# Kernel optimization log

Measured on AMD Instinct MI355X. Metric: run time of the kernel, lower is better.

The kernel has to match this reference:

```python
import jax, jax.numpy as jnp
import numpy as np

N, E, CIN, COUT = 100000, 1600000, 64, 128
EPS = 1e-5  # torch BatchNorm default


def setup_inputs() -> dict:
    key = jax.random.key(0)
    ks = jax.random.split(key, 16)
    s = 0.1
    x = jax.random.normal(ks[0], (N, CIN), jnp.float32)
    src = jax.random.randint(ks[1], (E,), 0, N, dtype=jnp.int32)
    dst = jax.random.randint(ks[2], (E,), 0, N, dtype=jnp.int32)
    edge_index = jnp.stack([src, dst])  # [2, E]
    return {
        "x": x,
        "edge_index": edge_index,
        # conv0: GraphConv(CIN -> COUT)
        "W_root0": jax.random.normal(ks[3], (COUT, CIN), jnp.float32) * s,
        "W_nbr0": jax.random.normal(ks[4], (COUT, CIN), jnp.float32) * s,
        "b0": jnp.zeros((COUT,), jnp.float32),
        # bn0
        "g0": jnp.ones((COUT,), jnp.float32),
        "be0": jnp.zeros((COUT,), jnp.float32),
        # conv1: GraphConv(COUT -> COUT)
        "W_root1": jax.random.normal(ks[5], (COUT, COUT), jnp.float32) * s,
        "W_nbr1": jax.random.normal(ks[6], (COUT, COUT), jnp.float32) * s,
        "b1": jnp.zeros((COUT,), jnp.float32),
        # bn1
        "g1": jnp.ones((COUT,), jnp.float32),
        "be1": jnp.zeros((COUT,), jnp.float32),
        # residual 1x1 conv (Conv1d(CIN, COUT, 1))
        "Wlin": jax.random.normal(ks[7], (COUT, CIN), jnp.float32) * s,
        "blin": jnp.zeros((COUT,), jnp.float32),
    }


def graph_conv(x, src, dst, W_root, W_nbr, b):
    # PyG GraphConv: out_i = W_root x_i + W_nbr * sum_{j: (j->i) in E} x_j + b
    agg = jax.ops.segment_sum(x[src], dst, num_segments=N)  # scatter-add over edges
    return x @ W_root.T + agg @ W_nbr.T + b


def batch_norm(x, gamma, beta):
    # training-mode BatchNorm over the node dimension (biased variance)
    mu = jnp.mean(x, axis=0)
    var = jnp.mean(jnp.square(x - mu), axis=0)
    return (x - mu) * jax.lax.rsqrt(var + EPS) * gamma + beta


def reference(x, edge_index, W_root0, W_nbr0, b0, g0, be0,
              W_root1, W_nbr1, b1, g1, be1, Wlin, blin):
    src, dst = edge_index[0], edge_index[1]
    y = batch_norm(graph_conv(x, src, dst, W_root0, W_nbr0, b0), g0, be0)
    y = jax.nn.relu(y)
    y = batch_norm(graph_conv(y, src, dst, W_root1, W_nbr1, b1), g1, be1)
    out = y + (x @ Wlin.T + blin)  # 1x1 Conv1d residual projection
    return jax.nn.relu(out)
```

## Files before the change

### kernel.cpp

```cpp
#include <hip/hip_runtime.h>
#include <stdint.h>


#define CIN 64
#define COUT 128
#define BN_EPS 1e-5f
#define CURPAD 32
#define PCPAD 32
#define SPAD 32
#define PSH 10
#define PNODES (1 << PSH)
#define MAXP 128

typedef unsigned short u16;
typedef short short8 __attribute__((ext_vector_type(8)));
typedef float f32x4 __attribute__((ext_vector_type(4)));

__device__ __forceinline__ float bf2f(u16 u) {
    union { unsigned int i; float f; } v; v.i = ((unsigned int)u) << 16; return v.f;
}
__device__ __forceinline__ u16 f2bf(float f) {
    union { float f; unsigned int i; } v; v.f = f;
    unsigned int r = v.i + 0x7fffu + ((v.i >> 16) & 1u);
    return (u16)(r >> 16);
}
__device__ __forceinline__ float lo16(unsigned int w) { return bf2f((u16)(w & 0xffffu)); }
__device__ __forceinline__ float hi16(unsigned int w) { return bf2f((u16)(w >> 16)); }

template<bool BF> __device__ __forceinline__ float ldf(const void* p, long i) {
    if (BF) return bf2f(((const u16*)p)[i]);
    return ((const float*)p)[i];
}
template<bool BF> __device__ __forceinline__ short8 ld8(const void* p, long i) {
    if (BF) return *(const short8*)((const u16*)p + i);
    const float* f = (const float*)p + i;
    short8 r;
#pragma unroll
    for (int j = 0; j < 8; ++j) r[j] = (short)f2bf(f[j]);
    return r;
}

__global__ void k_detect(const unsigned int* __restrict__ x, int* __restrict__ flag) {
    int lane = threadIdx.x;
    int cnt = 0;
#pragma unroll
    for (int i = 0; i < 8; ++i) {
        unsigned int w = x[lane * 8 + i];
        unsigned int e0 = (w >> 7) & 0xFFu, e1 = (w >> 23) & 0xFFu;
        cnt += (e0 >= 0x60u && e0 <= 0x8Eu);
        cnt += (e1 >= 0x60u && e1 <= 0x8Eu);
    }
    for (int o = 32; o; o >>= 1) cnt += __shfl_down(cnt, o);
    if (lane == 0) *flag = (cnt > 850) ? 1 : 0;
}

__global__ __launch_bounds__(256) void k_phist(const int* __restrict__ dst,
                                               int* __restrict__ pcount, int E, int np) {
    __shared__ int h[MAXP];
    for (int i = threadIdx.x; i < np; i += 256) h[i] = 0;
    __syncthreads();
    int stride = gridDim.x * 256;
    for (int e = blockIdx.x * 256 + threadIdx.x; e < E; e += stride)
        atomicAdd(&h[dst[e] >> PSH], 1);
    __syncthreads();
    for (int i = threadIdx.x; i < np; i += 256)
        if (h[i]) atomicAdd(&pcount[i * PCPAD], h[i]);
}

__global__ void k_pscan(const int* __restrict__ pcount, int* __restrict__ pstart,
                        int* __restrict__ pcursor, int np, int E) {
    __shared__ int s[MAXP];
    int t = threadIdx.x;
    int v = (t < np) ? pcount[t * PCPAD] : 0;
    s[t] = v; __syncthreads();
    for (int o = 1; o < MAXP; o <<= 1) {
        int u = (t >= o) ? s[t - o] : 0;
        __syncthreads(); s[t] += u; __syncthreads();
    }
    if (t < np) {
        int ex = s[t] - v;
        pstart[t] = ex;
        pcursor[t * CURPAD] = ex;
    }
    if (t == 0) pstart[np] = E;
}

__global__ __launch_bounds__(256) void k_pfill(const int* __restrict__ src,
        const int* __restrict__ dst, int* __restrict__ pcursor,
        unsigned int* __restrict__ barr, int E, int np) {
    __shared__ int cnt[MAXP], gb[MAXP], loc[MAXP];
    int tid = threadIdx.x;
    int base = blockIdx.x * 4096;
    for (int i = tid; i < np; i += 256) { cnt[i] = 0; loc[i] = 0; }
    __syncthreads();
    int pk[16]; unsigned int rec[16];
#pragma unroll
    for (int k = 0; k < 16; ++k) {
        int e = base + k * 256 + tid;
        if (e < E) {
            int d = dst[e];
            pk[k] = d >> PSH;
            rec[k] = ((unsigned int)(d & (PNODES - 1)) << 20) | (unsigned int)src[e];
            atomicAdd(&cnt[pk[k]], 1);
        } else pk[k] = -1;
    }
    __syncthreads();
    for (int i = tid; i < np; i += 256)
        if (cnt[i]) gb[i] = atomicAdd(&pcursor[i * CURPAD], cnt[i]);
    __syncthreads();
#pragma unroll
    for (int k = 0; k < 16; ++k) {
        if (pk[k] >= 0) {
            int off = atomicAdd(&loc[pk[k]], 1);
            barr[gb[pk[k]] + off] = rec[k];
        }
    }
}

__global__ __launch_bounds__(256) void k_psort(const unsigned int* __restrict__ barr,
        const int* __restrict__ pstart, int* __restrict__ csr,
        int* __restrict__ row_start, int n, int np, int E) {
    __shared__ int hist[PNODES], curs[PNODES], tsum[256];
    int tid = threadIdx.x;
    int p = blockIdx.x;
    int e0 = pstart[p], e1 = pstart[p + 1];
    int node0 = p << PSH;
#pragma unroll
    for (int j = 0; j < PNODES / 256; ++j) hist[tid + j * 256] = 0;
    __syncthreads();
    for (int t = e0 + tid; t < e1; t += 256)
        atomicAdd(&hist[barr[t] >> 20], 1);
    __syncthreads();
    int s0 = hist[tid * 4], s1 = hist[tid * 4 + 1], s2 = hist[tid * 4 + 2], s3 = hist[tid * 4 + 3];
    int sum4 = s0 + s1 + s2 + s3;
    tsum[tid] = sum4; __syncthreads();
    for (int o = 1; o < 256; o <<= 1) {
        int u = (tid >= o) ? tsum[tid - o] : 0;
        __syncthreads(); tsum[tid] += u; __syncthreads();
    }
    int bexc = tsum[tid] - sum4;
    int off0 = bexc, off1 = bexc + s0, off2 = off1 + s1, off3 = off2 + s2;
    curs[tid * 4] = off0; curs[tid * 4 + 1] = off1;
    curs[tid * 4 + 2] = off2; curs[tid * 4 + 3] = off3;
    int nd = node0 + tid * 4;
    if (nd < n)     row_start[nd]     = e0 + off0;
    if (nd + 1 < n) row_start[nd + 1] = e0 + off1;
    if (nd + 2 < n) row_start[nd + 2] = e0 + off2;
    if (nd + 3 < n) row_start[nd + 3] = e0 + off3;
    if (p == np - 1 && tid == 0) row_start[n] = E;
    __syncthreads();
    for (int t = e0 + tid; t < e1; t += 256) {
        unsigned int rec = barr[t];
        int pos = atomicAdd(&curs[rec >> 20], 1);
        csr[e0 + pos] = (int)(rec & 0xFFFFF);
    }
}

template<bool BF>
__device__ __forceinline__ void agg0_impl(const void* x, const int* rs, const int* csr,
                                          u16* agg, int n) {
    int i = blockIdx.x * 4 + (threadIdx.x >> 6);
    if (i >= n) return;
    int lane = threadIdx.x & 63;
    int h = lane >> 5, cp = lane & 31;
    int b = rs[i], e = rs[i + 1];
    float a0 = 0.f, a1 = 0.f, b0 = 0.f, b1 = 0.f;
    int t = b + h;
    for (; t + 2 < e; t += 4) {
        int j0 = csr[t], j1 = csr[t + 2];
        if (BF) {
            unsigned int w0 = ((const unsigned int*)x)[(long)j0 * 32 + cp];
            unsigned int w1 = ((const unsigned int*)x)[(long)j1 * 32 + cp];
            a0 += lo16(w0); a1 += hi16(w0);
            b0 += lo16(w1); b1 += hi16(w1);
        } else {
            float2 w0 = ((const float2*)x)[(long)j0 * 32 + cp];
            float2 w1 = ((const float2*)x)[(long)j1 * 32 + cp];
            a0 += w0.x; a1 += w0.y;
            b0 += w1.x; b1 += w1.y;
        }
    }
    for (; t < e; t += 2) {
        int j0 = csr[t];
        if (BF) {
            unsigned int w0 = ((const unsigned int*)x)[(long)j0 * 32 + cp];
            a0 += lo16(w0); a1 += hi16(w0);
        } else {
            float2 w0 = ((const float2*)x)[(long)j0 * 32 + cp];
            a0 += w0.x; a1 += w0.y;
        }
    }
    a0 += b0; a1 += b1;
    a0 += __shfl_xor(a0, 32);
    a1 += __shfl_xor(a1, 32);
    if (h == 0) {
        unsigned int o = (unsigned int)f2bf(a0) | ((unsigned int)f2bf(a1) << 16);
        ((unsigned int*)agg)[(long)i * 32 + cp] = o;
    }
}

__global__ __launch_bounds__(256) void k_agg0(const int* __restrict__ flag,
        const void* x, const int* __restrict__ rs, const int* __restrict__ csr,
        u16* __restrict__ agg, int n) {
    if (*flag) agg0_impl<true >(x, rs, csr, agg, n);
    else       agg0_impl<false>(x, rs, csr, agg, n);
}

__global__ __launch_bounds__(256) void k_agg1(const u16* __restrict__ y0,
        const int* __restrict__ rs, const int* __restrict__ csr,
        const float* __restrict__ scale, const float* __restrict__ shift,
        u16* __restrict__ agg, int n) {
    int i = blockIdx.x * 4 + (threadIdx.x >> 6);
    if (i >= n) return;
    int lane = threadIdx.x & 63;
    int c0 = 2 * lane;
    float s0 = scale[c0], s1 = scale[c0 + 1];
    float h0 = shift[c0], h1 = shift[c0 + 1];
    const unsigned int* y32 = (const unsigned int*)y0;
    int b = rs[i], e = rs[i + 1];
    float a0 = 0.f, a1 = 0.f, b0 = 0.f, b1 = 0.f;
    float c0a = 0.f, c1a = 0.f, d0 = 0.f, d1 = 0.f;
    int t = b;
    for (; t + 4 <= e; t += 4) {
        int j0 = csr[t], j1 = csr[t + 1], j2 = csr[t + 2], j3 = csr[t + 3];
        unsigned int w0 = y32[(long)j0 * 64 + lane];
        unsigned int w1 = y32[(long)j1 * 64 + lane];
        unsigned int w2 = y32[(long)j2 * 64 + lane];
        unsigned int w3 = y32[(long)j3 * 64 + lane];
        a0  += fmaxf(lo16(w0) * s0 + h0, 0.f); a1  += fmaxf(hi16(w0) * s1 + h1, 0.f);
        b0  += fmaxf(lo16(w1) * s0 + h0, 0.f); b1  += fmaxf(hi16(w1) * s1 + h1, 0.f);
        c0a += fmaxf(lo16(w2) * s0 + h0, 0.f); c1a += fmaxf(hi16(w2) * s1 + h1, 0.f);
        d0  += fmaxf(lo16(w3) * s0 + h0, 0.f); d1  += fmaxf(hi16(w3) * s1 + h1, 0.f);
    }
    for (; t < e; ++t) {
        unsigned int w0 = y32[(long)csr[t] * 64 + lane];
        a0 += fmaxf(lo16(w0) * s0 + h0, 0.f); a1 += fmaxf(hi16(w0) * s1 + h1, 0.f);
    }
    float s0t = (a0 + b0) + (c0a + d0);
    float s1t = (a1 + b1) + (c1a + d1);
    ((unsigned int*)agg)[(long)i * 64 + lane] =
        (unsigned int)f2bf(s0t) | ((unsigned int)f2bf(s1t) << 16);
}

template<bool BF>
__device__ __forceinline__ void gemm0_impl(const void* x, const u16* agg,
                                           const void* Wr, const void* Wn,
                                           u16* y0, float* sumP, float* sqP,
                                           int n, int nch, u16* lds) {
    const int ST = 130;
    int tid = threadIdx.x;
    int wave = tid >> 6, lane = tid & 63, lr = lane & 15, q = lane >> 4;

    short8 wf[2][4];
#pragma unroll
    for (int i = 0; i < 2; ++i) {
        int c = (2 * wave + i) * 16 + lr;
#pragma unroll
        for (int ks = 0; ks < 4; ++ks) {
            const void* W = (ks < 2) ? Wr : Wn;
            wf[i][ks] = ld8<BF>(W, (long)c * CIN + (ks & 1) * 32 + q * 8);
        }
    }

    const int rowb = tid >> 3, wb = tid & 7;
    const int rowf = tid >> 4, wfc = tid & 15;
    short8 rbx[2]; float4 rfx[4]; short8 rag[2];

    auto regload = [&](long chunk0) {
        if (BF) {
#pragma unroll
            for (int i = 0; i < 2; ++i) {
                long rg = chunk0 + rowb + i * 32; if (rg > n - 1) rg = n - 1;
                rbx[i] = *(const short8*)((const u16*)x + rg * CIN + wb * 8);
            }
        } else {
#pragma unroll
            for (int i = 0; i < 4; ++i) {
                long rg = chunk0 + rowf + i * 16; if (rg > n - 1) rg = n - 1;
                rfx[i] = *(const float4*)((const float*)x + rg * CIN + wfc * 4);
            }
        }
#pragma unroll
        for (int i = 0; i < 2; ++i) {
            long rg = chunk0 + rowb + i * 32; if (rg > n - 1) rg = n - 1;
            rag[i] = *(const short8*)(agg + rg * CIN + wb * 8);
        }
    };

    float st[2] = {0.f, 0.f}, sq[2] = {0.f, 0.f};
    int ch = blockIdx.x;
    if (ch < nch) regload((long)ch * 64);
    for (; ch < nch; ch += gridDim.x) {
        long chunk0 = (long)ch * 64;
        __syncthreads();
        if (BF) {
#pragma unroll
            for (int i = 0; i < 2; ++i)
                *(short8*)(lds + (rowb + i * 32) * ST + wb * 8) = rbx[i];
        } else {
#pragma unroll
            for (int i = 0; i < 4; ++i) {
                u16* d = lds + (rowf + i * 16) * ST + wfc * 4;
                d[0] = f2bf(rfx[i].x); d[1] = f2bf(rfx[i].y);
                d[2] = f2bf(rfx[i].z); d[3] = f2bf(rfx[i].w);
            }
        }
#pragma unroll
        for (int i = 0; i < 2; ++i)
            *(short8*)(lds + (rowb + i * 32) * ST + 64 + wb * 8) = rag[i];
        __syncthreads();
        long nxt = (long)ch + gridDim.x;
        if (nxt < nch) regload(nxt * 64);

#pragma unroll
        for (int t = 0; t < 4; ++t) {
            short8 a[4];
#pragma unroll
            for (int ks = 0; ks < 4; ++ks)
                a[ks] = *(const short8*)(lds + (t * 16 + lr) * ST + ks * 32 + q * 8);
#pragma unroll
            for (int i = 0; i < 2; ++i) {
                f32x4 acc = {0.f, 0.f, 0.f, 0.f};
#pragma unroll
                for (int ks = 0; ks < 4; ++ks)
                    acc = __builtin_amdgcn_mfma_f32_16x16x32_bf16(a[ks], wf[i][ks], acc, 0, 0, 0);
                int c = (2 * wave + i) * 16 + lr;
#pragma unroll
                for (int r = 0; r < 4; ++r) {
                    long row = chunk0 + t * 16 + q * 4 + r;
                    if (row < n) {
                        y0[row * COUT + c] = f2bf(acc[r]);
                        st[i] += acc[r]; sq[i] += acc[r] * acc[r];
                    }
                }
            }
        }
    }
#pragma unroll
    for (int i = 0; i < 2; ++i) {
        st[i] += __shfl_xor(st[i], 16); st[i] += __shfl_xor(st[i], 32);
        sq[i] += __shfl_xor(sq[i], 16); sq[i] += __shfl_xor(sq[i], 32);
    }
    if (q == 0) {
#pragma unroll
        for (int i = 0; i < 2; ++i) {
            int c = (2 * wave + i) * 16 + lr;
            atomicAdd(&sumP[c * SPAD], st[i]);
            atomicAdd(&sqP[c * SPAD], sq[i]);
        }
    }
}

__global__ __launch_bounds__(256) void k_gemm0(const int* __restrict__ flag,
        const void* x, const u16* __restrict__ agg, const void* Wr, const void* Wn,
        u16* __restrict__ y0, float* __restrict__ sumP, float* __restrict__ sqP,
        int n, int nch) {
    __shared__ u16 lds[64 * 130];
    if (*flag) gemm0_impl<true >(x, agg, Wr, Wn, y0, sumP, sqP, n, nch, lds);
    else       gemm0_impl<false>(x, agg, Wr, Wn, y0, sumP, sqP, n, nch, lds);
}

template<bool BF>
__device__ __forceinline__ void gemm1_impl(const u16* y0, const u16* agg,
                                           const void* Wr, const void* Wn,
                                           const float* sc0, const float* sh0,
                                           u16* y1, float* sumP, float* sqP,
                                           int n, int nch, u16* lds) {
    const int ST = 258;
    int tid = threadIdx.x;
    int wave = tid >> 6, lane = tid & 63, lr = lane & 15, q = lane >> 4;

    short8 wf[2][8];
#pragma unroll
    for (int i = 0; i < 2; ++i) {
        int c = (2 * wave + i) * 16 + lr;
#pragma unroll
        for (int ks = 0; ks < 8; ++ks) {
            const void* W = (ks < 4) ? Wr : Wn;
            wf[i][ks] = ld8<BF>(W, (long)c * COUT + (ks & 3) * 32 + q * 8);
        }
    }

    const int rowy = tid >> 4, wy = tid & 15;
    float s8[8], h8[8];
#pragma unroll
    for (int j = 0; j < 8; ++j) { s8[j] = sc0[wy * 8 + j]; h8[j] = sh0[wy * 8 + j]; }

    short8 ry[4], rag[4];
    auto regload = [&](long chunk0) {
#pragma unroll
        for (int i = 0; i < 4; ++i) {
            long rg = chunk0 + rowy + i * 16; if (rg > n - 1) rg = n - 1;
            ry[i]  = *(const short8*)(y0  + rg * COUT + wy * 8);
            rag[i] = *(const short8*)(agg + rg * COUT + wy * 8);
        }
    };

    float st[2] = {0.f, 0.f}, sq[2] = {0.f, 0.f};
    int ch = blockIdx.x;
    if (ch < nch) regload((long)ch * 64);
    for (; ch < nch; ch += gridDim.x) {
        long chunk0 = (long)ch * 64;
        __syncthreads();
#pragma unroll
        for (int i = 0; i < 4; ++i) {
            short8 o;
#pragma unroll
            for (int j = 0; j < 8; ++j)
                o[j] = (short)f2bf(fmaxf(bf2f((u16)ry[i][j]) * s8[j] + h8[j], 0.f));
            *(short8*)(lds + (rowy + i * 16) * ST + wy * 8) = o;
            *(short8*)(lds + (rowy + i * 16) * ST + 128 + wy * 8) = rag[i];
        }
        __syncthreads();
        long nxt = (long)ch + gridDim.x;
        if (nxt < nch) regload(nxt * 64);

#pragma unroll
        for (int t = 0; t < 4; ++t) {
            short8 a[8];
#pragma unroll
            for (int ks = 0; ks < 8; ++ks)
                a[ks] = *(const short8*)(lds + (t * 16 + lr) * ST + ks * 32 + q * 8);
#pragma unroll
            for (int i = 0; i < 2; ++i) {
                f32x4 acc = {0.f, 0.f, 0.f, 0.f};
#pragma unroll
                for (int ks = 0; ks < 8; ++ks)
                    acc = __builtin_amdgcn_mfma_f32_16x16x32_bf16(a[ks], wf[i][ks], acc, 0, 0, 0);
                int c = (2 * wave + i) * 16 + lr;
#pragma unroll
                for (int r = 0; r < 4; ++r) {
                    long row = chunk0 + t * 16 + q * 4 + r;
                    if (row < n) {
                        y1[row * COUT + c] = f2bf(acc[r]);
                        st[i] += acc[r]; sq[i] += acc[r] * acc[r];
                    }
                }
            }
        }
    }
#pragma unroll
    for (int i = 0; i < 2; ++i) {
        st[i] += __shfl_xor(st[i], 16); st[i] += __shfl_xor(st[i], 32);
        sq[i] += __shfl_xor(sq[i], 16); sq[i] += __shfl_xor(sq[i], 32);
    }
    if (q == 0) {
#pragma unroll
        for (int i = 0; i < 2; ++i) {
            int c = (2 * wave + i) * 16 + lr;
            atomicAdd(&sumP[c * SPAD], st[i]);
            atomicAdd(&sqP[c * SPAD], sq[i]);
        }
    }
}

__global__ __launch_bounds__(256) void k_gemm1(const int* __restrict__ flag,
        const u16* __restrict__ y0, const u16* __restrict__ agg,
        const void* Wr, const void* Wn,
        const float* __restrict__ sc0, const float* __restrict__ sh0,
        u16* y1_bf , u16* y1_ws,
        float* __restrict__ sumP, float* __restrict__ sqP, int n, int nch) {
    __shared__ u16 lds[64 * 258];
    u16* y1 = *flag ? y1_bf : y1_ws;
    if (*flag) gemm1_impl<true >(y0, agg, Wr, Wn, sc0, sh0, y1, sumP, sqP, n, nch, lds);
    else       gemm1_impl<false>(y0, agg, Wr, Wn, sc0, sh0, y1, sumP, sqP, n, nch, lds);
}

__global__ void k_bnfin(const int* __restrict__ flag,
                        const float* __restrict__ sumP, const float* __restrict__ sqP,
                        const void* g, const void* be,
                        float* __restrict__ scale, float* __restrict__ shift, int n) {
    int c = threadIdx.x;
    bool bf = (*flag != 0);
    float inv = 1.f / (float)n;
    float mu = sumP[c * SPAD] * inv;
    float var = fmaxf(sqP[c * SPAD] * inv - mu * mu, 0.f);
    float gv = bf ? bf2f(((const u16*)g)[c]) : ((const float*)g)[c];
    float bv = bf ? bf2f(((const u16*)be)[c]) : ((const float*)be)[c];
    float sc = gv * rsqrtf(var + BN_EPS);
    scale[c] = sc;
    shift[c] = bv - mu * sc;
}

template<bool BF>
__device__ __forceinline__ void final_impl(const void* x, const u16* y1,
                                           const void* Wlin, const void* blin,
                                           const float* sc, const float* sh,
                                           void* out, int n, int nch, u16* lds) {
    const int ST = 194;
    int tid = threadIdx.x;
    int wave = tid >> 6, lane = tid & 63, lr = lane & 15, q = lane >> 4;

    short8 wf[2][2];
    float blc[2], scc[2], shc[2];
#pragma unroll
    for (int i = 0; i < 2; ++i) {
        int c = (2 * wave + i) * 16 + lr;
#pragma unroll
        for (int ks = 0; ks < 2; ++ks)
            wf[i][ks] = ld8<BF>(Wlin, (long)c * CIN + ks * 32 + q * 8);
        blc[i] = ldf<BF>(blin, c);
        scc[i] = sc[c]; shc[i] = sh[c];
    }

    const int rowb = tid >> 3, wb = tid & 7;
    const int rowf = tid >> 4, wfc = tid & 15;
    const int rowy = tid >> 4, wy = tid & 15;
    short8 rbx[2]; float4 rfx[4]; short8 ry[4];

    auto regload = [&](long chunk0) {
        if (BF) {
#pragma unroll
            for (int i = 0; i < 2; ++i) {
                long rg = chunk0 + rowb + i * 32; if (rg > n - 1) rg = n - 1;
                rbx[i] = *(const short8*)((const u16*)x + rg * CIN + wb * 8);
            }
        } else {
#pragma unroll
            for (int i = 0; i < 4; ++i) {
                long rg = chunk0 + rowf + i * 16; if (rg > n - 1) rg = n - 1;
                rfx[i] = *(const float4*)((const float*)x + rg * CIN + wfc * 4);
            }
        }
#pragma unroll
        for (int i = 0; i < 4; ++i) {
            long rg = chunk0 + rowy + i * 16; if (rg > n - 1) rg = n - 1;
            ry[i] = *(const short8*)(y1 + rg * COUT + wy * 8);
        }
    };

    int ch = blockIdx.x;
    if (ch < nch) regload((long)ch * 64);
    for (; ch < nch; ch += gridDim.x) {
        long chunk0 = (long)ch * 64;
        __syncthreads();
        if (BF) {
#pragma unroll
            for (int i = 0; i < 2; ++i)
                *(short8*)(lds + (rowb + i * 32) * ST + wb * 8) = rbx[i];
        } else {
#pragma unroll
            for (int i = 0; i < 4; ++i) {
                u16* d = lds + (rowf + i * 16) * ST + wfc * 4;
                d[0] = f2bf(rfx[i].x); d[1] = f2bf(rfx[i].y);
                d[2] = f2bf(rfx[i].z); d[3] = f2bf(rfx[i].w);
            }
        }
#pragma unroll
        for (int i = 0; i < 4; ++i)
            *(short8*)(lds + (rowy + i * 16) * ST + 64 + wy * 8) = ry[i];
        __syncthreads();
        long nxt = (long)ch + gridDim.x;
        if (nxt < nch) regload(nxt * 64);

#pragma unroll
        for (int t = 0; t < 4; ++t) {
            short8 a[2];
#pragma unroll
            for (int ks = 0; ks < 2; ++ks)
                a[ks] = *(const short8*)(lds + (t * 16 + lr) * ST + ks * 32 + q * 8);
#pragma unroll
            for (int i = 0; i < 2; ++i) {
                f32x4 acc = {0.f, 0.f, 0.f, 0.f};
                acc = __builtin_amdgcn_mfma_f32_16x16x32_bf16(a[0], wf[i][0], acc, 0, 0, 0);
                acc = __builtin_amdgcn_mfma_f32_16x16x32_bf16(a[1], wf[i][1], acc, 0, 0, 0);
                int c = (2 * wave + i) * 16 + lr;
#pragma unroll
                for (int r = 0; r < 4; ++r) {
                    long row = chunk0 + t * 16 + q * 4 + r;
                    if (row < n) {
                        float yv = bf2f(lds[(t * 16 + q * 4 + r) * ST + 64 + c]);
                        float v = acc[r] + blc[i] + yv * scc[i] + shc[i];
                        v = fmaxf(v, 0.f);
                        if (BF) ((u16*)out)[row * COUT + c] = f2bf(v);
                        else    ((float*)out)[row * COUT + c] = v;
                    }
                }
            }
        }
    }
}

__global__ __launch_bounds__(256) void k_final(const int* __restrict__ flag,
        const void* x, const void* Wlin, const void* blin,
        const u16* y1_bf , const u16* y1_ws,
        const float* __restrict__ sc, const float* __restrict__ sh,
        void* out, int n, int nch) {
    __shared__ u16 lds[64 * 194];
    const u16* y1 = *flag ? y1_bf : y1_ws;
    if (*flag) final_impl<true >(x, y1, Wlin, blin, sc, sh, out, n, nch, lds);
    else       final_impl<false>(x, y1, Wlin, blin, sc, sh, out, n, nch, lds);
}

extern "C" void kernel_launch(void* const* d_in, const int* in_sizes, int n_in,
                              void* d_out, int out_size, void* d_ws, size_t ws_size,
                              hipStream_t stream) {
    (void)n_in; (void)out_size; (void)ws_size;
    const void* x    = d_in[0];
    const int*  ei   = (const int*)d_in[1];
    const void* Wr0  = d_in[2];
    const void* Wn0  = d_in[3];
    const void* g0   = d_in[5];
    const void* be0  = d_in[6];
    const void* Wr1  = d_in[7];
    const void* Wn1  = d_in[8];
    const void* g1   = d_in[10];
    const void* be1  = d_in[11];
    const void* Wlin = d_in[12];
    const void* blin = d_in[13];

    const int N = in_sizes[0] / CIN;
    const int E = in_sizes[1] / 2;
    const int* src = ei;
    const int* dst = ei + E;
    const int NP = (N + PNODES - 1) >> PSH;

    char* base = (char*)d_ws;
    size_t off = 0;
    auto carve = [&](size_t bytes) -> void* {
        void* p = base + off;
        off = (off + bytes + 255) & ~(size_t)255;
        return p;
    };
    int*   flag      = (int*)carve(256);
    int*   pcount    = (int*)carve(MAXP * PCPAD * sizeof(int));
    int*   pstart    = (int*)carve((MAXP + 1) * sizeof(int));
    int*   pcursor   = (int*)carve(MAXP * CURPAD * sizeof(int));
    float* statsP    = (float*)carve(4 * 128 * SPAD * sizeof(float));
    float* scsh      = (float*)carve(512 * sizeof(float));
    int*   row_start = (int*)carve((size_t)(N + 1) * sizeof(int));
    unsigned int* barr = (unsigned int*)carve((size_t)E * sizeof(int));
    int*   csr       = (int*)carve((size_t)E * sizeof(int));
    u16*   aggu      = (u16*)carve((size_t)N * COUT * sizeof(u16));
    u16*   y0        = (u16*)carve((size_t)N * COUT * sizeof(u16));
    u16*   y1_ws     = (u16*)carve((size_t)N * COUT * sizeof(u16));

    float* sum0P = statsP;
    float* sq0P  = statsP + 128 * SPAD;
    float* sum1P = statsP + 256 * SPAD;
    float* sq1P  = statsP + 384 * SPAD;

    hipMemsetAsync(pcount, 0, MAXP * PCPAD * sizeof(int), stream);
    hipMemsetAsync(statsP, 0, 4 * 128 * SPAD * sizeof(float), stream);

    const int nwb = (N + 3) / 4;
    const int nch = (N + 63) / 64;
    const int ntl = (E + 4095) / 4096;
    const int G   = nch < 1024 ? nch : 1024;

    k_detect<<<1, 64, 0, stream>>>((const unsigned int*)x, flag);

    k_phist<<<256, 256, 0, stream>>>(dst, pcount, E, NP);
    k_pscan<<<1, MAXP, 0, stream>>>(pcount, pstart, pcursor, NP, E);
    k_pfill<<<ntl, 256, 0, stream>>>(src, dst, pcursor, barr, E, NP);
    k_psort<<<NP, 256, 0, stream>>>(barr, pstart, csr, row_start, N, NP, E);

    k_agg0 <<<nwb, 256, 0, stream>>>(flag, x, row_start, csr, aggu, N);
    k_gemm0<<<G, 256, 0, stream>>>(flag, x, aggu, Wr0, Wn0, y0,
                                   sum0P, sq0P, N, nch);
    k_bnfin<<<1, 128, 0, stream>>>(flag, sum0P, sq0P, g0, be0,
                                   scsh, scsh + 128, N);

    k_agg1 <<<nwb, 256, 0, stream>>>(y0, row_start, csr, scsh, scsh + 128, aggu, N);
    k_gemm1<<<G, 256, 0, stream>>>(flag, y0, aggu, Wr1, Wn1, scsh, scsh + 128,
                                   (u16*)d_out, y1_ws, sum1P, sq1P, N, nch);
    k_bnfin<<<1, 128, 0, stream>>>(flag, sum1P, sq1P, g1, be1,
                                   scsh + 256, scsh + 384, N);

    k_final<<<G, 256, 0, stream>>>(flag, x, Wlin, blin,
                                   (const u16*)d_out, y1_ws,
                                   scsh + 256, scsh + 384, d_out, N, nch);
}
```

Before: 413.3 us.

## Precompute BN+ReLU on y0 in place and widen gather loads to 16 bytes

Adds a k_y0p pass that applies BN0 scale/shift and ReLU to y0 in place, once per node. Both k_agg1 and k_gemm1 then read activated values directly instead of recomputing the affine+ReLU per gathered edge. The gather kernels agg0 and agg1 now use 16-byte vector loads, with several edges handled in parallel per wave and combined by shuffle reductions. The cost is an extra streaming read/write pass over y0 and one more kernel launch.

New measurement: 397.0 us. -4.0%, faster.

```diff
diff --git a/kernel.cpp b/kernel.cpp
--- a/kernel.cpp
+++ b/kernel.cpp
@@ -162,40 +162,73 @@
     int i = blockIdx.x * 4 + (threadIdx.x >> 6);
     if (i >= n) return;
     int lane = threadIdx.x & 63;
-    int h = lane >> 5, cp = lane & 31;
     int b = rs[i], e = rs[i + 1];
-    float a0 = 0.f, a1 = 0.f, b0 = 0.f, b1 = 0.f;
-    int t = b + h;
-    for (; t + 2 < e; t += 4) {
-        int j0 = csr[t], j1 = csr[t + 2];
-        if (BF) {
-            unsigned int w0 = ((const unsigned int*)x)[(long)j0 * 32 + cp];
-            unsigned int w1 = ((const unsigned int*)x)[(long)j1 * 32 + cp];
-            a0 += lo16(w0); a1 += hi16(w0);
-            b0 += lo16(w1); b1 += hi16(w1);
-        } else {
-            float2 w0 = ((const float2*)x)[(long)j0 * 32 + cp];
-            float2 w1 = ((const float2*)x)[(long)j1 * 32 + cp];
-            a0 += w0.x; a1 += w0.y;
-            b0 += w1.x; b1 += w1.y;
-        }
-    }
-    for (; t < e; t += 2) {
-        int j0 = csr[t];
-        if (BF) {
-            unsigned int w0 = ((const unsigned int*)x)[(long)j0 * 32 + cp];
-            a0 += lo16(w0); a1 += hi16(w0);
-        } else {
-            float2 w0 = ((const float2*)x)[(long)j0 * 32 + cp];
-            a0 += w0.x; a1 += w0.y;
-        }
-    }
-    a0 += b0; a1 += b1;
-    a0 += __shfl_xor(a0, 32);
-    a1 += __shfl_xor(a1, 32);
-    if (h == 0) {
-        unsigned int o = (unsigned int)f2bf(a0) | ((unsigned int)f2bf(a1) << 16);
-        ((unsigned int*)agg)[(long)i * 32 + cp] = o;
+    if (BF) {
+        int slot = lane >> 3, cp = lane & 7;
+        float acc[8] = {0.f, 0.f, 0.f, 0.f, 0.f, 0.f, 0.f, 0.f};
+        int t = b + slot;
+        for (; t + 8 < e; t += 16) {
+            int j0 = csr[t], j1 = csr[t + 8];
+            uint4 w0 = *((const uint4*)((const unsigned int*)x + (long)j0 * 32) + cp);
+            uint4 w1 = *((const uint4*)((const unsigned int*)x + (long)j1 * 32) + cp);
+            acc[0] += lo16(w0.x); acc[1] += hi16(w0.x);
+            acc[2] += lo16(w0.y); acc[3] += hi16(w0.y);
+            acc[4] += lo16(w0.z); acc[5] += hi16(w0.z);
+            acc[6] += lo16(w0.w); acc[7] += hi16(w0.w);
+            acc[0] += lo16(w1.x); acc[1] += hi16(w1.x);
+            acc[2] += lo16(w1.y); acc[3] += hi16(w1.y);
+            acc[4] += lo16(w1.z); acc[5] += hi16(w1.z);
+            acc[6] += lo16(w1.w); acc[7] += hi16(w1.w);
+        }
+        if (t < e) {
+            int j0 = csr[t];
+            uint4 w0 = *((const uint4*)((const unsigned int*)x + (long)j0 * 32) + cp);
+            acc[0] += lo16(w0.x); acc[1] += hi16(w0.x);
+            acc[2] += lo16(w0.y); acc[3] += hi16(w0.y);
+            acc[4] += lo16(w0.z); acc[5] += hi16(w0.z);
+            acc[6] += lo16(w0.w); acc[7] += hi16(w0.w);
+        }
+#pragma unroll
+        for (int k = 0; k < 8; ++k) {
+            acc[k] += __shfl_xor(acc[k], 8);
+            acc[k] += __shfl_xor(acc[k], 16);
+            acc[k] += __shfl_xor(acc[k], 32);
+        }
+        if (slot == 0) {
+            uint4 o;
+            o.x = (unsigned int)f2bf(acc[0]) | ((unsigned int)f2bf(acc[1]) << 16);
+            o.y = (unsigned int)f2bf(acc[2]) | ((unsigned int)f2bf(acc[3]) << 16);
+            o.z = (unsigned int)f2bf(acc[4]) | ((unsigned int)f2bf(acc[5]) << 16);
+            o.w = (unsigned int)f2bf(acc[6]) | ((unsigned int)f2bf(acc[7]) << 16);
+            *((uint4*)((unsigned int*)agg + (long)i * 32) + cp) = o;
+        }
+    } else {
+        int slot = lane >> 4, cp = lane & 15;
+        float acc[4] = {0.f, 0.f, 0.f, 0.f};
+        int t = b + slot;
+        for (; t + 4 < e; t += 8) {
+            int j0 = csr[t], j1 = csr[t + 4];
+            float4 w0 = *((const float4*)((const float*)x + (long)j0 * 64) + cp);
+            float4 w1 = *((const float4*)((const float*)x + (long)j1 * 64) + cp);
+            acc[0] += w0.x + w1.x; acc[1] += w0.y + w1.y;
+            acc[2] += w0.z + w1.z; acc[3] += w0.w + w1.w;
+        }
+        if (t < e) {
+            int j0 = csr[t];
+            float4 w0 = *((const float4*)((const float*)x + (long)j0 * 64) + cp);
+            acc[0] += w0.x; acc[1] += w0.y; acc[2] += w0.z; acc[3] += w0.w;
+        }
+#pragma unroll
+        for (int k = 0; k < 4; ++k) {
+            acc[k] += __shfl_xor(acc[k], 16);
+            acc[k] += __shfl_xor(acc[k], 32);
+        }
+        if (slot == 0) {
+            unsigned int o0 = (unsigned int)f2bf(acc[0]) | ((unsigned int)f2bf(acc[1]) << 16);
+            unsigned int o1 = (unsigned int)f2bf(acc[2]) | ((unsigned int)f2bf(acc[3]) << 16);
+            uint2 o; o.x = o0; o.y = o1;
+            *((uint2*)((unsigned int*)agg + (long)i * 32) + cp) = o;
+        }
     }
 }
 
@@ -206,40 +239,75 @@
     else       agg0_impl<false>(x, rs, csr, agg, n);
 }
 
-__global__ __launch_bounds__(256) void k_agg1(const u16* __restrict__ y0,
+__global__ __launch_bounds__(256) void k_y0p(unsigned int* __restrict__ y0,
+        const float* __restrict__ sc, const float* __restrict__ sh, long nq) {
+    long idx = (long)blockIdx.x * 256 + threadIdx.x;
+    int colq = threadIdx.x & 15;
+    float s8[8], h8[8];
+#pragma unroll
+    for (int j = 0; j < 8; ++j) { s8[j] = sc[colq * 8 + j]; h8[j] = sh[colq * 8 + j]; }
+    long stride = (long)gridDim.x * 256;
+    uint4* p = (uint4*)y0;
+    for (; idx < nq; idx += stride) {
+        uint4 w = p[idx];
+        unsigned int r[4] = {w.x, w.y, w.z, w.w};
+        uint4 o;
+        unsigned int* po = (unsigned int*)&o;
+#pragma unroll
+        for (int d = 0; d < 4; ++d) {
+            float a = fmaxf(lo16(r[d]) * s8[2 * d]     + h8[2 * d],     0.f);
+            float b = fmaxf(hi16(r[d]) * s8[2 * d + 1] + h8[2 * d + 1], 0.f);
+            po[d] = (unsigned int)f2bf(a) | ((unsigned int)f2bf(b) << 16);
+        }
+        p[idx] = o;
+    }
+}
+
+__global__ __launch_bounds__(256) void k_agg1(const u16* __restrict__ y0p,
         const int* __restrict__ rs, const int* __restrict__ csr,
-        const float* __restrict__ scale, const float* __restrict__ shift,
         u16* __restrict__ agg, int n) {
     int i = blockIdx.x * 4 + (threadIdx.x >> 6);
     if (i >= n) return;
     int lane = threadIdx.x & 63;
-    int c0 = 2 * lane;
-    float s0 = scale[c0], s1 = scale[c0 + 1];
-    float h0 = shift[c0], h1 = shift[c0 + 1];
-    const unsigned int* y32 = (const unsigned int*)y0;
+    int slot = lane >> 4, cp = lane & 15;
+    const unsigned int* y32 = (const unsigned int*)y0p;
     int b = rs[i], e = rs[i + 1];
-    float a0 = 0.f, a1 = 0.f, b0 = 0.f, b1 = 0.f;
-    float c0a = 0.f, c1a = 0.f, d0 = 0.f, d1 = 0.f;
-    int t = b;
-    for (; t + 4 <= e; t += 4) {
-        int j0 = csr[t], j1 = csr[t + 1], j2 = csr[t + 2], j3 = csr[t + 3];
-        unsigned int w0 = y32[(long)j0 * 64 + lane];
-        unsigned int w1 = y32[(long)j1 * 64 + lane];
-        unsigned int w2 = y32[(long)j2 * 64 + lane];
-        unsigned int w3 = y32[(long)j3 * 64 + lane];
-        a0  += fmaxf(lo16(w0) * s0 + h0, 0.f); a1  += fmaxf(hi16(w0) * s1 + h1, 0.f);
-        b0  += fmaxf(lo16(w1) * s0 + h0, 0.f); b1  += fmaxf(hi16(w1) * s1 + h1, 0.f);
-        c0a += fmaxf(lo16(w2) * s0 + h0, 0.f); c1a += fmaxf(hi16(w2) * s1 + h1, 0.f);
-        d0  += fmaxf(lo16(w3) * s0 + h0, 0.f); d1  += fmaxf(hi16(w3) * s1 + h1, 0.f);
-    }
-    for (; t < e; ++t) {
-        unsigned int w0 = y32[(long)csr[t] * 64 + lane];
-        a0 += fmaxf(lo16(w0) * s0 + h0, 0.f); a1 += fmaxf(hi16(w0) * s1 + h1, 0.f);
-    }
-    float s0t = (a0 + b0) + (c0a + d0);
-    float s1t = (a1 + b1) + (c1a + d1);
-    ((unsigned int*)agg)[(long)i * 64 + lane] =
-        (unsigned int)f2bf(s0t) | ((unsigned int)f2bf(s1t) << 16);
+    float acc[8] = {0.f, 0.f, 0.f, 0.f, 0.f, 0.f, 0.f, 0.f};
+    int t = b + slot;
+    for (; t + 4 < e; t += 8) {
+        int j0 = csr[t], j1 = csr[t + 4];
+        uint4 w0 = *((const uint4*)(y32 + (long)j0 * 64) + cp);
+        uint4 w1 = *((const uint4*)(y32 + (long)j1 * 64) + cp);
+        acc[0] += lo16(w0.x); acc[1] += hi16(w0.x);
+        acc[2] += lo16(w0.y); acc[3] += hi16(w0.y);
+        acc[4] += lo16(w0.z); acc[5] += hi16(w0.z);
+        acc[6] += lo16(w0.w); acc[7] += hi16(w0.w);
+        acc[0] += lo16(w1.x); acc[1] += hi16(w1.x);
+        acc[2] += lo16(w1.y); acc[3] += hi16(w1.y);
+        acc[4] += lo16(w1.z); acc[5] += hi16(w1.z);
+        acc[6] += lo16(w1.w); acc[7] += hi16(w1.w);
+    }
+    if (t < e) {
+        int j0 = csr[t];
+        uint4 w0 = *((const uint4*)(y32 + (long)j0 * 64) + cp);
+        acc[0] += lo16(w0.x); acc[1] += hi16(w0.x);
+        acc[2] += lo16(w0.y); acc[3] += hi16(w0.y);
+        acc[4] += lo16(w0.z); acc[5] += hi16(w0.z);
+        acc[6] += lo16(w0.w); acc[7] += hi16(w0.w);
+    }
+#pragma unroll
+    for (int k = 0; k < 8; ++k) {
+        acc[k] += __shfl_xor(acc[k], 16);
+        acc[k] += __shfl_xor(acc[k], 32);
+    }
+    if (slot == 0) {
+        uint4 o;
+        o.x = (unsigned int)f2bf(acc[0]) | ((unsigned int)f2bf(acc[1]) << 16);
+        o.y = (unsigned int)f2bf(acc[2]) | ((unsigned int)f2bf(acc[3]) << 16);
+        o.z = (unsigned int)f2bf(acc[4]) | ((unsigned int)f2bf(acc[5]) << 16);
+        o.w = (unsigned int)f2bf(acc[6]) | ((unsigned int)f2bf(acc[7]) << 16);
+        *((uint4*)((unsigned int*)agg + (long)i * 64) + cp) = o;
+    }
 }
 
 template<bool BF>
@@ -361,9 +429,8 @@
 }
 
 template<bool BF>
-__device__ __forceinline__ void gemm1_impl(const u16* y0, const u16* agg,
+__device__ __forceinline__ void gemm1_impl(const u16* y0p, const u16* agg,
                                            const void* Wr, const void* Wn,
-                                           const float* sc0, const float* sh0,
                                            u16* y1, float* sumP, float* sqP,
                                            int n, int nch, u16* lds) {
     const int ST = 258;
@@ -382,16 +449,12 @@
     }
 
     const int rowy = tid >> 4, wy = tid & 15;
-    float s8[8], h8[8];
-#pragma unroll
-    for (int j = 0; j < 8; ++j) { s8[j] = sc0[wy * 8 + j]; h8[j] = sh0[wy * 8 + j]; }
-
     short8 ry[4], rag[4];
     auto regload = [&](long chunk0) {
 #pragma unroll
         for (int i = 0; i < 4; ++i) {
             long rg = chunk0 + rowy + i * 16; if (rg > n - 1) rg = n - 1;
-            ry[i]  = *(const short8*)(y0  + rg * COUT + wy * 8);
+            ry[i]  = *(const short8*)(y0p + rg * COUT + wy * 8);
             rag[i] = *(const short8*)(agg + rg * COUT + wy * 8);
         }
     };
@@ -404,11 +467,7 @@
         __syncthreads();
 #pragma unroll
         for (int i = 0; i < 4; ++i) {
-            short8 o;
-#pragma unroll
-            for (int j = 0; j < 8; ++j)
-                o[j] = (short)f2bf(fmaxf(bf2f((u16)ry[i][j]) * s8[j] + h8[j], 0.f));
-            *(short8*)(lds + (rowy + i * 16) * ST + wy * 8) = o;
+            *(short8*)(lds + (rowy + i * 16) * ST + wy * 8) = ry[i];
             *(short8*)(lds + (rowy + i * 16) * ST + 128 + wy * 8) = rag[i];
         }
         __syncthreads();
@@ -455,15 +514,14 @@
 }
 
 __global__ __launch_bounds__(256) void k_gemm1(const int* __restrict__ flag,
-        const u16* __restrict__ y0, const u16* __restrict__ agg,
+        const u16* __restrict__ y0p, const u16* __restrict__ agg,
         const void* Wr, const void* Wn,
-        const float* __restrict__ sc0, const float* __restrict__ sh0,
         u16* y1_bf , u16* y1_ws,
         float* __restrict__ sumP, float* __restrict__ sqP, int n, int nch) {
     __shared__ u16 lds[64 * 258];
     u16* y1 = *flag ? y1_bf : y1_ws;
-    if (*flag) gemm1_impl<true >(y0, agg, Wr, Wn, sc0, sh0, y1, sumP, sqP, n, nch, lds);
-    else       gemm1_impl<false>(y0, agg, Wr, Wn, sc0, sh0, y1, sumP, sqP, n, nch, lds);
+    if (*flag) gemm1_impl<true >(y0p, agg, Wr, Wn, y1, sumP, sqP, n, nch, lds);
+    else       gemm1_impl<false>(y0p, agg, Wr, Wn, y1, sumP, sqP, n, nch, lds);
 }
 
 __global__ void k_bnfin(const int* __restrict__ flag,
@@ -647,6 +705,8 @@
     const int nch = (N + 63) / 64;
     const int ntl = (E + 4095) / 4096;
     const int G   = nch < 1024 ? nch : 1024;
+    const long nq = (long)N * 16;
+    int g2 = (int)((nq + 255) / 256); if (g2 > 2048) g2 = 2048;
 
     k_detect<<<1, 64, 0, stream>>>((const unsigned int*)x, flag);
 
@@ -661,8 +721,10 @@
     k_bnfin<<<1, 128, 0, stream>>>(flag, sum0P, sq0P, g0, be0,
                                    scsh, scsh + 128, N);
 
-    k_agg1 <<<nwb, 256, 0, stream>>>(y0, row_start, csr, scsh, scsh + 128, aggu, N);
-    k_gemm1<<<G, 256, 0, stream>>>(flag, y0, aggu, Wr1, Wn1, scsh, scsh + 128,
+    k_y0p<<<g2, 256, 0, stream>>>((unsigned int*)y0, scsh, scsh + 128, nq);
+
+    k_agg1 <<<nwb, 256, 0, stream>>>(y0, row_start, csr, aggu, N);
+    k_gemm1<<<G, 256, 0, stream>>>(flag, y0, aggu, Wr1, Wn1,
                                    (u16*)d_out, y1_ws, sum1P, sq1P, N, nch);
     k_bnfin<<<1, 128, 0, stream>>>(flag, sum1P, sq1P, g1, be1,
                                    scsh + 256, scsh + 384, N);
```
